# Performance work log

Measured on AMD Instinct MI355X. Metric: run time of the kernel, lower is better.

## Reference

```python
import jax, jax.numpy as jnp
import numpy as np
from jax import lax


def _sobel_kernels3d(n1=1, n2=2, n3=2):
    Sx = np.asarray([[[-n1, 0, n1], [-n2, 0, n2], [-n1, 0, n1]],
                     [[-n2, 0, n2], [-n3 * n2, 0, n3 * n2], [-n2, 0, n2]],
                     [[-n1, 0, n1], [-n2, 0, n2], [-n1, 0, n1]]])
    Sy = np.asarray([[[-n1, -n2, -n1], [0, 0, 0], [n1, n2, n1]],
                     [[-n2, -n3 * n2, -n2], [0, 0, 0], [n2, n3 * n2, n2]],
                     [[-n1, -n2, -n1], [0, 0, 0], [n1, n2, n1]]])
    Sz = np.asarray([[[-n1, -n2, -n1], [-n2, -n3 * n2, -n2], [-n1, -n2, -n1]],
                     [[0, 0, 0], [0, 0, 0], [0, 0, 0]],
                     [[n1, n2, n1], [n2, n3 * n2, n2], [n1, n2, n1]]])
    Sd11 = np.asarray([[[0, n1, n2], [-n1, 0, n1], [-n2, -n1, 0]],
                       [[0, n2, n2 * n3], [-n2, 0, n2], [-n2 * n3, -n2, 0]],
                       [[0, n1, n2], [-n1, 0, n1], [-n2, -n1, 0]]])
    Sd12 = np.asarray([[[-n2, -n1, 0], [-n1, 0, n1], [0, n1, n2]],
                       [[-n2 * n3, -n2, 0], [-n2, 0, n2], [0, n2, n2 * n3]],
                       [[-n2, -n1, 0], [-n1, 0, n1], [0, n1, n2]]])
    Sd21 = Sd11.T
    Sd22 = Sd12.T
    Sd31 = np.asarray([-S.T for S in Sd11.T])
    Sd32 = np.asarray([S.T for S in Sd12.T])
    S = [Sx, Sy, Sz, Sd11, Sd12, Sd21, Sd22, Sd31, Sd32]
    # (9, 1, 3, 3, 3) OIDHW conv weight bank
    return np.stack(S).astype(np.float32)[:, None]


def _grad_edge3d(img, kernels, a=1):
    # img: (B, C, H, W, D); kernels: (9, 1, 3, 3, 3)
    B, C, H, W, D = img.shape
    p = jnp.pad(img, ((0, 0), (0, 0), (a, a), (a, a), (a, a)), mode='reflect')
    Hp, Wp, Dp = H + 2 * a, W + 2 * a, D + 2 * a
    # Each channel convolved independently with all 9 kernels in one conv call.
    xin = p.reshape(B * C, 1, Hp, Wp, Dp)
    conv = lax.conv_general_dilated(
        xin, kernels, window_strides=(1, 1, 1), padding='SAME',
        dimension_numbers=('NCDHW', 'OIDHW', 'NCDHW'))  # (B*C, 9, Hp, Wp, Dp)
    conv = conv.reshape(B, C, 9, Hp, Wp, Dp)
    # torch: sum_c (conv + 1e-6), squared per-filter, then sum_s (. + 1e-6), sqrt, * 1/C
    per_filter = jnp.sum(conv + 1e-6, axis=1)           # (B, 9, Hp, Wp, Dp)
    mag = jnp.sqrt(jnp.sum(per_filter ** 2, axis=1) + 9 * 1e-6) / C  # (B, Hp, Wp, Dp)
    mag = mag[:, a:-a, a:-a, a:-a]                      # (B, H, W, D)
    mn = mag.min()
    mx = mag.max()
    norm = (mag - mn) / (mx - mn + 1e-6)
    return norm.reshape(B, 1, H, W, D)


def setup_inputs() -> dict:
    key = jax.random.key(0)
    kx, ky = jax.random.split(key)
    B, C, H, W, D = 4, 1, 128, 128, 128
    x = jax.random.normal(kx, (B, C, H, W, D), dtype=jnp.float32)
    y = jax.random.normal(ky, (B, C, H, W, D), dtype=jnp.float32)
    kernels = jnp.asarray(_sobel_kernels3d(1, 2, 2))
    return {"x": x, "y": y, "kernels": kernels}


def reference(x, y, kernels):
    edge_x = _grad_edge3d(x, kernels)
    edge_y = _grad_edge3d(y, kernels)
    # lam_errors = [(1.0, L1Loss())], reduction='sum' -> 1e-6 + 1.0 * mean|ex-ey|
    l1 = jnp.mean(jnp.abs(edge_x - edge_y))
    return 1e-6 + 1.0 * l1
```

## Files before the change

kernel.cpp:

```cpp
#include <hip/hip_runtime.h>
#include <hip/hip_fp16.h>

#define HH 128
#define NB 4
#define NVOX (NB * HH * HH * HH)

#define NBLK1 4096
#define GRID2 512
#define TPB 256

__device__ __align__(16) unsigned int g_bmin[NBLK1];
__device__ __align__(16) unsigned int g_bmax[NBLK1];

union U4H8 { uint4 u; __half2 h[4]; };

__global__ __launch_bounds__(256) void pass1_kernel(
    const float* __restrict__ x, const float* __restrict__ y,
    __half* __restrict__ magx, __half* __restrict__ magy,
    float* __restrict__ out) {
    int bid = blockIdx.x;
    int tid = threadIdx.x;
    if (bid == 0 && tid == 0) out[0] = 0.0f;

    int lane = tid & 63, wid = tid >> 6;
    int wg  = bid & 31;
    int ck  = (bid >> 5) & 1;
    int hs  = (bid >> 6) & 7;
    int b   = (bid >> 9) & 3;
    int img = bid >> 11;

    const float* __restrict__ src = img ? y : x;
    __half* __restrict__ dst = img ? magy : magx;

    int w  = wg * 4 + wid;
    int wm = (w == 0) ? 1 : (w - 1);
    int wp = (w == 127) ? 126 : (w + 1);
    int d0 = ck << 6;
    int h0 = hs << 4;
    bool ck0 = (ck == 0);
    const float* base = src + ((size_t)b << 21) + d0;

    float sbD[3], ubD[3], dbS[3], sbS[3], ubS[3], dbU[3], sbU[3];
    float mn = 3.4e38f, mx = 0.0f;

    auto cstage = [&](float q, float E, float& S, float& D, float& U) {
        float qls = __shfl_up(q, 1);
        float qrs = __shfl_down(q, 1);
        float q1  = __shfl(q, 1);
        float q62 = __shfl(q, 62);
        float qL = (lane == 0)  ? (ck0 ? q1 : E) : qls;
        float qR = (lane == 63) ? (ck0 ? E : q62) : qrs;
        float t = qL + qR;
        S = fmaf(2.0f, q, t);
        D = qR - qL;
        U = t + q;
    };

#pragma unroll
    for (int r = 0; r < 18; ++r) {
        int hr = h0 + r - 1;
        hr = (hr < 0) ? 1 : ((hr > 127) ? 126 : hr);
        const float* rm = base + (((hr << 7) + wm) << 7);
        const float* rc = base + (((hr << 7) + w)  << 7);
        const float* rp = base + (((hr << 7) + wp) << 7);
        float qm = rm[lane], qc = rc[lane], qp = rp[lane];
        float em = ck0 ? rm[64] : rm[-1];
        float ec = ck0 ? rc[64] : rc[-1];
        float ep = ck0 ? rp[64] : rp[-1];

        float S0, D0, U0, S1, D1, U1, S2, D2, U2;
        cstage(qm, em, S0, D0, U0);
        cstage(qc, ec, S1, D1, U1);
        cstage(qp, ep, S2, D2, U2);

        int slot = r % 3;
        float tD = D0 + D2;
        sbD[slot] = fmaf(2.0f, D1, tD);
        ubD[slot] = tD + D1;
        float tS = S0 + S2;
        sbS[slot] = fmaf(2.0f, S1, tS);
        ubS[slot] = tS + S1;
        dbS[slot] = S2 - S0;
        float tU = U0 + U2;
        sbU[slot] = fmaf(2.0f, U1, tU);
        dbU[slot] = U2 - U0;

        if (r >= 2) {
            int s0 = (r - 2) % 3, s1 = (r - 1) % 3, s2 = slot;

            float tsbD = sbD[s0] + sbD[s2];
            float Gssd = fmaf(2.0f, sbD[s1], tsbD);
            float Gusd = tsbD + sbD[s1];
            float tubD = ubD[s0] + ubD[s2];
            float Gsud = fmaf(2.0f, ubD[s1], tubD);
            float tdbS = dbS[s0] + dbS[s2];
            float Gsds = fmaf(2.0f, dbS[s1], tdbS);
            float Guds = tdbS + dbS[s1];
            float Gdss = sbS[s2] - sbS[s0];
            float Gdus = ubS[s2] - ubS[s0];
            float tdbU = dbU[s0] + dbU[s2];
            float Gsdu = fmaf(2.0f, dbU[s1], tdbU);
            float Gdsu = sbU[s2] - sbU[s0];

            float f0 = Gssd;
            float f1 = Gsds;
            float f2 = Gdss;
            float f3 = Gsud - Gsdu;
            float f4 = Gsud + Gsdu;
            float f5 = Gdus - Guds;
            float f6 = Gdus + Guds;
            float f7 = Gusd - Gdsu;
            float f8 = Gusd + Gdsu;

            const float e1 = 1e-6f;
            float s = 9.0f * 1e-6f;
            float u;
            u = f0 + e1; s = fmaf(u, u, s);
            u = f1 + e1; s = fmaf(u, u, s);
            u = f2 + e1; s = fmaf(u, u, s);
            u = f3 + e1; s = fmaf(u, u, s);
            u = f4 + e1; s = fmaf(u, u, s);
            u = f5 + e1; s = fmaf(u, u, s);
            u = f6 + e1; s = fmaf(u, u, s);
            u = f7 + e1; s = fmaf(u, u, s);
            u = f8 + e1; s = fmaf(u, u, s);
            float m = sqrtf(s);

            __half hm = __float2half_rn(m);
            float m2 = __half2float(hm);
            int hout = h0 + r - 2;
            int idx = (((b * 128 + hout) * 128 + w) << 7) + d0 + lane;
            __builtin_nontemporal_store(__half_as_ushort(hm), (unsigned short*)&dst[idx]);
            mn = fminf(mn, m2);
            mx = fmaxf(mx, m2);
        }
    }

    unsigned int umn = __float_as_uint(mn);
    unsigned int umx = __float_as_uint(mx);
#pragma unroll
    for (int off = 32; off > 0; off >>= 1) {
        unsigned int a1 = __shfl_down(umn, off, 64);
        unsigned int b1 = __shfl_down(umx, off, 64);
        umn = (a1 < umn) ? a1 : umn;
        umx = (b1 > umx) ? b1 : umx;
    }
    __shared__ unsigned int smn[4], smx[4];
    if (lane == 0) { smn[wid] = umn; smx[wid] = umx; }
    __syncthreads();
    if (tid == 0) {
        unsigned int m0 = smn[0] < smn[1] ? smn[0] : smn[1];
        unsigned int m1 = smn[2] < smn[3] ? smn[2] : smn[3];
        unsigned int x0 = smx[0] > smx[1] ? smx[0] : smx[1];
        unsigned int x1 = smx[2] > smx[3] ? smx[2] : smx[3];
        g_bmin[bid] = (m0 < m1 ? m0 : m1);
        g_bmax[bid] = (x0 > x1 ? x0 : x1);
    }
}

__global__ __launch_bounds__(TPB) void pass2_kernel(
    const uint4* __restrict__ magx8, const uint4* __restrict__ magy8,
    float* __restrict__ out) {
    int tid = threadIdx.x, bid = blockIdx.x;
    int lane = tid & 63, wid = tid >> 6;
    __shared__ unsigned int sred[4][4];
    __shared__ float smm[4];
    __shared__ float sv[4];

    const uint4* bmin4 = (const uint4*)g_bmin;
    const uint4* bmax4 = (const uint4*)g_bmax;
    unsigned int v0 = 0xFFFFFFFFu, v1 = 0u, v2 = 0xFFFFFFFFu, v3 = 0u;
#pragma unroll
    for (int k = 0; k < 2; ++k) {
        int i = k * TPB + tid;
        uint4 a = bmin4[i];
        uint4 b = bmax4[i];
        uint4 c = bmin4[i + 512];
        uint4 d = bmax4[i + 512];
        unsigned int a01 = (a.x < a.y) ? a.x : a.y, a23 = (a.z < a.w) ? a.z : a.w;
        unsigned int b01 = (b.x > b.y) ? b.x : b.y, b23 = (b.z > b.w) ? b.z : b.w;
        unsigned int c01 = (c.x < c.y) ? c.x : c.y, c23 = (c.z < c.w) ? c.z : c.w;
        unsigned int d01 = (d.x > d.y) ? d.x : d.y, d23 = (d.z > d.w) ? d.z : d.w;
        unsigned int ar = (a01 < a23) ? a01 : a23;
        unsigned int br = (b01 > b23) ? b01 : b23;
        unsigned int cr = (c01 < c23) ? c01 : c23;
        unsigned int dr = (d01 > d23) ? d01 : d23;
        v0 = (ar < v0) ? ar : v0;
        v1 = (br > v1) ? br : v1;
        v2 = (cr < v2) ? cr : v2;
        v3 = (dr > v3) ? dr : v3;
    }
#pragma unroll
    for (int off = 32; off > 0; off >>= 1) {
        unsigned int a0 = __shfl_down(v0, off, 64);
        unsigned int a1 = __shfl_down(v1, off, 64);
        unsigned int a2 = __shfl_down(v2, off, 64);
        unsigned int a3 = __shfl_down(v3, off, 64);
        v0 = (a0 < v0) ? a0 : v0;
        v1 = (a1 > v1) ? a1 : v1;
        v2 = (a2 < v2) ? a2 : v2;
        v3 = (a3 > v3) ? a3 : v3;
    }
    if (lane == 0) { sred[wid][0] = v0; sred[wid][1] = v1; sred[wid][2] = v2; sred[wid][3] = v3; }
    __syncthreads();
    if (tid == 0) {
        unsigned int r0 = sred[0][0], r1 = sred[0][1], r2 = sred[0][2], r3 = sred[0][3];
#pragma unroll
        for (int w = 1; w < 4; ++w) {
            r0 = (sred[w][0] < r0) ? sred[w][0] : r0;
            r1 = (sred[w][1] > r1) ? sred[w][1] : r1;
            r2 = (sred[w][2] < r2) ? sred[w][2] : r2;
            r3 = (sred[w][3] > r3) ? sred[w][3] : r3;
        }
        smm[0] = __uint_as_float(r0);
        smm[1] = __uint_as_float(r1);
        smm[2] = __uint_as_float(r2);
        smm[3] = __uint_as_float(r3);
    }
    __syncthreads();

    float mnx = smm[0], mxx = smm[1], mny = smm[2], mxy = smm[3];
    float ix = 1.0f / (mxx - mnx + 1e-6f);
    float iy = 1.0f / (mxy - mny + 1e-6f);
    float cx = -mnx * ix;
    float cy = -mny * iy;

    float s = 0.0f;
#pragma unroll
    for (int k = 0; k < 8; ++k) {
        int i = bid * 2048 + k * TPB + tid;
        U4H8 qa, qb;
        qa.u = magx8[i];
        qb.u = magy8[i];
#pragma unroll
        for (int j = 0; j < 4; ++j) {
            float2 va = __half22float2(qa.h[j]);
            float2 vb = __half22float2(qb.h[j]);
            s += fabsf(fmaf(va.x, ix, cx) - fmaf(vb.x, iy, cy));
            s += fabsf(fmaf(va.y, ix, cx) - fmaf(vb.y, iy, cy));
        }
    }
#pragma unroll
    for (int off = 32; off > 0; off >>= 1) s += __shfl_down(s, off, 64);
    if (lane == 0) sv[wid] = s;
    __syncthreads();
    if (tid == 0) {
        float partial = ((sv[0] + sv[1]) + (sv[2] + sv[3])) * (1.0f / (float)NVOX);
        if (bid == 0) partial += 1e-6f;
        atomicAdd(out, partial);
    }
}

extern "C" void kernel_launch(void* const* d_in, const int* in_sizes, int n_in,
                              void* d_out, int out_size, void* d_ws, size_t ws_size,
                              hipStream_t stream) {
    const float* x = (const float*)d_in[0];
    const float* y = (const float*)d_in[1];
    float* out = (float*)d_out;

    __half* magx = (__half*)d_ws;
    __half* magy = magx + NVOX;

    pass1_kernel<<<NBLK1, 256, 0, stream>>>(x, y, magx, magy, out);
    pass2_kernel<<<GRID2, TPB, 0, stream>>>((const uint4*)magx, (const uint4*)magy, out);
}
```

Baseline: 142.9 us.

## Process full depth row per wavefront with float2 loads, halving pass1 blocks

Each lane in pass1 now handles two adjacent depth voxels through float2 loads, so one wavefront covers the whole 128-wide depth row. This removes the depth split into two chunks, along with the extra halo loads and chunk-boundary shuffles. Stores become packed half2 writes, the block count drops from 4096 to 2048, and pass2's min/max reduction is shrunk to match. Per-thread register pressure roughly doubles and there are fewer blocks to hide latency, which may reduce occupancy.

```diff
diff --git a/kernel.cpp b/kernel.cpp
--- a/kernel.cpp
+++ b/kernel.cpp
@@ -5,7 +5,7 @@
 #define NB 4
 #define NVOX (NB * HH * HH * HH)
 
-#define NBLK1 4096
+#define NBLK1 2048
 #define GRID2 512
 #define TPB 256
 
@@ -24,10 +24,9 @@
 
     int lane = tid & 63, wid = tid >> 6;
     int wg  = bid & 31;
-    int ck  = (bid >> 5) & 1;
-    int hs  = (bid >> 6) & 7;
-    int b   = (bid >> 9) & 3;
-    int img = bid >> 11;
+    int hs  = (bid >> 5) & 7;
+    int b   = (bid >> 8) & 3;
+    int img = bid >> 10;
 
     const float* __restrict__ src = img ? y : x;
     __half* __restrict__ dst = img ? magy : magx;
@@ -35,104 +34,126 @@
     int w  = wg * 4 + wid;
     int wm = (w == 0) ? 1 : (w - 1);
     int wp = (w == 127) ? 126 : (w + 1);
-    int d0 = ck << 6;
     int h0 = hs << 4;
-    bool ck0 = (ck == 0);
-    const float* base = src + ((size_t)b << 21) + d0;
-
-    float sbD[3], ubD[3], dbS[3], sbS[3], ubS[3], dbU[3], sbU[3];
+    const float2* base2 = (const float2*)(src + ((size_t)b << 21));
+
+    float2 sbD[3], ubD[3], dbS[3], sbS[3], ubS[3], dbU[3], sbU[3];
     float mn = 3.4e38f, mx = 0.0f;
-
-    auto cstage = [&](float q, float E, float& S, float& D, float& U) {
-        float qls = __shfl_up(q, 1);
-        float qrs = __shfl_down(q, 1);
-        float q1  = __shfl(q, 1);
-        float q62 = __shfl(q, 62);
-        float qL = (lane == 0)  ? (ck0 ? q1 : E) : qls;
-        float qR = (lane == 63) ? (ck0 ? E : q62) : qrs;
-        float t = qL + qR;
-        S = fmaf(2.0f, q, t);
-        D = qR - qL;
-        U = t + q;
+    bool l0 = (lane == 0), l63 = (lane == 63);
+
+    auto cstage = [&](float2 q, float2& S, float2& D, float2& U) {
+        float Lxs = __shfl_up(q.y, 1);
+        float Rys = __shfl_down(q.x, 1);
+        float Lx = l0  ? q.y : Lxs;
+        float Ry = l63 ? q.x : Rys;
+        float tx = Lx + q.y;
+        float ty = q.x + Ry;
+        S.x = fmaf(2.0f, q.x, tx);
+        S.y = fmaf(2.0f, q.y, ty);
+        D.x = q.y - Lx;
+        D.y = Ry - q.x;
+        U.x = tx + q.x;
+        U.y = ty + q.y;
     };
 
 #pragma unroll
     for (int r = 0; r < 18; ++r) {
         int hr = h0 + r - 1;
         hr = (hr < 0) ? 1 : ((hr > 127) ? 126 : hr);
-        const float* rm = base + (((hr << 7) + wm) << 7);
-        const float* rc = base + (((hr << 7) + w)  << 7);
-        const float* rp = base + (((hr << 7) + wp) << 7);
-        float qm = rm[lane], qc = rc[lane], qp = rp[lane];
-        float em = ck0 ? rm[64] : rm[-1];
-        float ec = ck0 ? rc[64] : rc[-1];
-        float ep = ck0 ? rp[64] : rp[-1];
-
-        float S0, D0, U0, S1, D1, U1, S2, D2, U2;
-        cstage(qm, em, S0, D0, U0);
-        cstage(qc, ec, S1, D1, U1);
-        cstage(qp, ep, S2, D2, U2);
+        const float2* rm = base2 + (((hr << 7) + wm) << 6);
+        const float2* rc = base2 + (((hr << 7) + w)  << 6);
+        const float2* rp = base2 + (((hr << 7) + wp) << 6);
+        float2 qm = rm[lane], qc = rc[lane], qp = rp[lane];
+
+        float2 S0, D0, U0, S1, D1, U1, S2, D2, U2;
+        cstage(qm, S0, D0, U0);
+        cstage(qc, S1, D1, U1);
+        cstage(qp, S2, D2, U2);
 
         int slot = r % 3;
-        float tD = D0 + D2;
-        sbD[slot] = fmaf(2.0f, D1, tD);
-        ubD[slot] = tD + D1;
-        float tS = S0 + S2;
-        sbS[slot] = fmaf(2.0f, S1, tS);
-        ubS[slot] = tS + S1;
-        dbS[slot] = S2 - S0;
-        float tU = U0 + U2;
-        sbU[slot] = fmaf(2.0f, U1, tU);
-        dbU[slot] = U2 - U0;
+        float2 tD = { D0.x + D2.x, D0.y + D2.y };
+        sbD[slot] = { fmaf(2.0f, D1.x, tD.x), fmaf(2.0f, D1.y, tD.y) };
+        ubD[slot] = { tD.x + D1.x, tD.y + D1.y };
+        float2 tS = { S0.x + S2.x, S0.y + S2.y };
+        sbS[slot] = { fmaf(2.0f, S1.x, tS.x), fmaf(2.0f, S1.y, tS.y) };
+        ubS[slot] = { tS.x + S1.x, tS.y + S1.y };
+        dbS[slot] = { S2.x - S0.x, S2.y - S0.y };
+        float2 tU = { U0.x + U2.x, U0.y + U2.y };
+        sbU[slot] = { fmaf(2.0f, U1.x, tU.x), fmaf(2.0f, U1.y, tU.y) };
+        dbU[slot] = { U2.x - U0.x, U2.y - U0.y };
 
         if (r >= 2) {
             int s0 = (r - 2) % 3, s1 = (r - 1) % 3, s2 = slot;
-
-            float tsbD = sbD[s0] + sbD[s2];
-            float Gssd = fmaf(2.0f, sbD[s1], tsbD);
-            float Gusd = tsbD + sbD[s1];
-            float tubD = ubD[s0] + ubD[s2];
-            float Gsud = fmaf(2.0f, ubD[s1], tubD);
-            float tdbS = dbS[s0] + dbS[s2];
-            float Gsds = fmaf(2.0f, dbS[s1], tdbS);
-            float Guds = tdbS + dbS[s1];
-            float Gdss = sbS[s2] - sbS[s0];
-            float Gdus = ubS[s2] - ubS[s0];
-            float tdbU = dbU[s0] + dbU[s2];
-            float Gsdu = fmaf(2.0f, dbU[s1], tdbU);
-            float Gdsu = sbU[s2] - sbU[s0];
-
-            float f0 = Gssd;
-            float f1 = Gsds;
-            float f2 = Gdss;
-            float f3 = Gsud - Gsdu;
-            float f4 = Gsud + Gsdu;
-            float f5 = Gdus - Guds;
-            float f6 = Gdus + Guds;
-            float f7 = Gusd - Gdsu;
-            float f8 = Gusd + Gdsu;
-
-            const float e1 = 1e-6f;
-            float s = 9.0f * 1e-6f;
-            float u;
-            u = f0 + e1; s = fmaf(u, u, s);
-            u = f1 + e1; s = fmaf(u, u, s);
-            u = f2 + e1; s = fmaf(u, u, s);
-            u = f3 + e1; s = fmaf(u, u, s);
-            u = f4 + e1; s = fmaf(u, u, s);
-            u = f5 + e1; s = fmaf(u, u, s);
-            u = f6 + e1; s = fmaf(u, u, s);
-            u = f7 + e1; s = fmaf(u, u, s);
-            u = f8 + e1; s = fmaf(u, u, s);
-            float m = sqrtf(s);
-
-            __half hm = __float2half_rn(m);
-            float m2 = __half2float(hm);
+            float2 m2;
+#pragma unroll
+            for (int c = 0; c < 2; ++c) {
+                float vsbD0 = c ? sbD[s0].y : sbD[s0].x;
+                float vsbD1 = c ? sbD[s1].y : sbD[s1].x;
+                float vsbD2 = c ? sbD[s2].y : sbD[s2].x;
+                float vubD0 = c ? ubD[s0].y : ubD[s0].x;
+                float vubD1 = c ? ubD[s1].y : ubD[s1].x;
+                float vubD2 = c ? ubD[s2].y : ubD[s2].x;
+                float vdbS0 = c ? dbS[s0].y : dbS[s0].x;
+                float vdbS1 = c ? dbS[s1].y : dbS[s1].x;
+                float vdbS2 = c ? dbS[s2].y : dbS[s2].x;
+                float vsbS0 = c ? sbS[s0].y : sbS[s0].x;
+                float vsbS2 = c ? sbS[s2].y : sbS[s2].x;
+                float vubS0 = c ? ubS[s0].y : ubS[s0].x;
+                float vubS2 = c ? ubS[s2].y : ubS[s2].x;
+                float vdbU0 = c ? dbU[s0].y : dbU[s0].x;
+                float vdbU1 = c ? dbU[s1].y : dbU[s1].x;
+                float vdbU2 = c ? dbU[s2].y : dbU[s2].x;
+                float vsbU0 = c ? sbU[s0].y : sbU[s0].x;
+                float vsbU2 = c ? sbU[s2].y : sbU[s2].x;
+
+                float tsbD = vsbD0 + vsbD2;
+                float Gssd = fmaf(2.0f, vsbD1, tsbD);
+                float Gusd = tsbD + vsbD1;
+                float tubD = vubD0 + vubD2;
+                float Gsud = fmaf(2.0f, vubD1, tubD);
+                float tdbS = vdbS0 + vdbS2;
+                float Gsds = fmaf(2.0f, vdbS1, tdbS);
+                float Guds = tdbS + vdbS1;
+                float Gdss = vsbS2 - vsbS0;
+                float Gdus = vubS2 - vubS0;
+                float tdbU = vdbU0 + vdbU2;
+                float Gsdu = fmaf(2.0f, vdbU1, tdbU);
+                float Gdsu = vsbU2 - vsbU0;
+
+                float f0 = Gssd;
+                float f1 = Gsds;
+                float f2 = Gdss;
+                float f3 = Gsud - Gsdu;
+                float f4 = Gsud + Gsdu;
+                float f5 = Gdus - Guds;
+                float f6 = Gdus + Guds;
+                float f7 = Gusd - Gdsu;
+                float f8 = Gusd + Gdsu;
+
+                const float e1 = 1e-6f;
+                float s = 9.0f * 1e-6f;
+                float u;
+                u = f0 + e1; s = fmaf(u, u, s);
+                u = f1 + e1; s = fmaf(u, u, s);
+                u = f2 + e1; s = fmaf(u, u, s);
+                u = f3 + e1; s = fmaf(u, u, s);
+                u = f4 + e1; s = fmaf(u, u, s);
+                u = f5 + e1; s = fmaf(u, u, s);
+                u = f6 + e1; s = fmaf(u, u, s);
+                u = f7 + e1; s = fmaf(u, u, s);
+                u = f8 + e1; s = fmaf(u, u, s);
+                float m = sqrtf(s);
+                if (c) m2.y = m; else m2.x = m;
+            }
+
+            __half2 hm2 = __float22half2_rn(m2);
+            float2 mr = __half22float2(hm2);
             int hout = h0 + r - 2;
-            int idx = (((b * 128 + hout) * 128 + w) << 7) + d0 + lane;
-            __builtin_nontemporal_store(__half_as_ushort(hm), (unsigned short*)&dst[idx]);
-            mn = fminf(mn, m2);
-            mx = fmaxf(mx, m2);
+            int h2idx = (((b * 128 + hout) * 128 + w) << 6) + lane;
+            __builtin_nontemporal_store(*(unsigned int*)&hm2,
+                (unsigned int*)((__half2*)dst + h2idx));
+            mn = fminf(mn, fminf(mr.x, mr.y));
+            mx = fmaxf(mx, fmaxf(mr.x, mr.y));
         }
     }
 
@@ -169,37 +190,28 @@
 
     const uint4* bmin4 = (const uint4*)g_bmin;
     const uint4* bmax4 = (const uint4*)g_bmax;
-    unsigned int v0 = 0xFFFFFFFFu, v1 = 0u, v2 = 0xFFFFFFFFu, v3 = 0u;
-#pragma unroll
-    for (int k = 0; k < 2; ++k) {
-        int i = k * TPB + tid;
-        uint4 a = bmin4[i];
-        uint4 b = bmax4[i];
-        uint4 c = bmin4[i + 512];
-        uint4 d = bmax4[i + 512];
-        unsigned int a01 = (a.x < a.y) ? a.x : a.y, a23 = (a.z < a.w) ? a.z : a.w;
-        unsigned int b01 = (b.x > b.y) ? b.x : b.y, b23 = (b.z > b.w) ? b.z : b.w;
-        unsigned int c01 = (c.x < c.y) ? c.x : c.y, c23 = (c.z < c.w) ? c.z : c.w;
-        unsigned int d01 = (d.x > d.y) ? d.x : d.y, d23 = (d.z > d.w) ? d.z : d.w;
-        unsigned int ar = (a01 < a23) ? a01 : a23;
-        unsigned int br = (b01 > b23) ? b01 : b23;
-        unsigned int cr = (c01 < c23) ? c01 : c23;
-        unsigned int dr = (d01 > d23) ? d01 : d23;
-        v0 = (ar < v0) ? ar : v0;
-        v1 = (br > v1) ? br : v1;
-        v2 = (cr < v2) ? cr : v2;
-        v3 = (dr > v3) ? dr : v3;
-    }
+    uint4 a = bmin4[tid];
+    uint4 b = bmax4[tid];
+    uint4 c = bmin4[tid + 256];
+    uint4 d = bmax4[tid + 256];
+    unsigned int a01 = (a.x < a.y) ? a.x : a.y, a23 = (a.z < a.w) ? a.z : a.w;
+    unsigned int b01 = (b.x > b.y) ? b.x : b.y, b23 = (b.z > b.w) ? b.z : b.w;
+    unsigned int c01 = (c.x < c.y) ? c.x : c.y, c23 = (c.z < c.w) ? c.z : c.w;
+    unsigned int d01 = (d.x > d.y) ? d.x : d.y, d23 = (d.z > d.w) ? d.z : d.w;
+    unsigned int v0 = (a01 < a23) ? a01 : a23;
+    unsigned int v1 = (b01 > b23) ? b01 : b23;
+    unsigned int v2 = (c01 < c23) ? c01 : c23;
+    unsigned int v3 = (d01 > d23) ? d01 : d23;
 #pragma unroll
     for (int off = 32; off > 0; off >>= 1) {
-        unsigned int a0 = __shfl_down(v0, off, 64);
-        unsigned int a1 = __shfl_down(v1, off, 64);
-        unsigned int a2 = __shfl_down(v2, off, 64);
-        unsigned int a3 = __shfl_down(v3, off, 64);
-        v0 = (a0 < v0) ? a0 : v0;
-        v1 = (a1 > v1) ? a1 : v1;
-        v2 = (a2 < v2) ? a2 : v2;
-        v3 = (a3 > v3) ? a3 : v3;
+        unsigned int t0 = __shfl_down(v0, off, 64);
+        unsigned int t1 = __shfl_down(v1, off, 64);
+        unsigned int t2 = __shfl_down(v2, off, 64);
+        unsigned int t3 = __shfl_down(v3, off, 64);
+        v0 = (t0 < v0) ? t0 : v0;
+        v1 = (t1 > v1) ? t1 : v1;
+        v2 = (t2 < v2) ? t2 : v2;
+        v3 = (t3 > v3) ? t3 : v3;
     }
     if (lane == 0) { sred[wid][0] = v0; sred[wid][1] = v1; sred[wid][2] = v2; sred[wid][3] = v3; }
     __syncthreads();
```

Result: no change. 143.3 us (+0.2%).
